# Kernel optimization log

Hardware: AMD Instinct MI355X
Metric: run time of the kernel (lower is better)

The kernel has to match this reference:

```python
import jax, jax.numpy as jnp
import numpy as np

B, L, HID, TRANS = 16384, 512, 768, 128


def setup_inputs() -> dict:
    key = jax.random.key(0)
    ks = jax.random.split(key, 12)
    def lin(k, out_d, in_d):
        kw, kb = jax.random.split(k)
        s = 1.0 / np.sqrt(in_d)
        return (jax.random.uniform(kw, (out_d, in_d), jnp.float32, -s, s),
                jax.random.uniform(kb, (out_d,), jnp.float32, -s, s))
    W_text, b_text = lin(ks[0], TRANS, HID)
    W_label, b_label = lin(ks[1], TRANS, HID)
    W0, b0 = lin(ks[2], TRANS, 2 * TRANS)
    W1, b1 = lin(ks[3], TRANS, TRANS)
    W2, b2 = lin(ks[4], 1, TRANS)
    target = jax.random.randint(ks[5], (B, L), 0, 2, jnp.int32)
    # guarantee every sample has at least one positive label (torch.mean on empty would NaN)
    target = target.at[:, 0].set(1)
    return {
        "text_embed": jax.random.normal(ks[6], (B, HID), jnp.float32),
        "label_embed": jax.random.normal(ks[7], (L, HID), jnp.float32),
        "target": target,
        "perm": jax.random.permutation(ks[8], B).astype(jnp.int32),
        "W_text": W_text, "b_text": b_text,
        "W_label": W_label, "b_label": b_label,
        "W0": W0, "b0": b0, "W1": W1, "b1": b1, "W2": W2, "b2": b2,
    }


def _network(t, l, W_text, b_text, W_label, b_label, W0, b0, W1, b1, W2, b2):
    tt = t @ W_text.T + b_text            # [B, trans]
    ll = l @ W_label.T + b_label          # [B, trans]
    h = jnp.concatenate([tt, ll], axis=1)  # [B, 2*trans]
    h = jax.nn.relu(h @ W0.T + b0)
    h = jax.nn.relu(h @ W1.T + b1)
    return h @ W2.T + b2                  # [B, 1]


def reference(text_embed, label_embed, target, perm,
              W_text, b_text, W_label, b_label, W0, b0, W1, b1, W2, b2):
    # variable-length mean pooling of label embeddings selected by the multi-hot target
    mask = target.astype(text_embed.dtype)                 # [B, L]
    counts = jnp.maximum(mask.sum(axis=1, keepdims=True), 1.0)
    label_feature_y = (mask @ label_embed) / counts        # [B, hid]
    negative_text = text_embed[perm]                       # shuffled negatives
    params = (W_text, b_text, W_label, b_label, W0, b0, W1, b1, W2, b2)
    E_joint = -jnp.mean(jax.nn.softplus(-_network(text_embed, label_feature_y, *params)))
    E_marginal = jnp.mean(jax.nn.softplus(_network(negative_text, label_feature_y, *params)))
    return E_marginal - E_joint
```

## Files before the change

### kernel.cpp

```cpp
#include <hip/hip_runtime.h>
#include <math.h>

#define BATCH 16384
#define LBL   512
#define HID   768
#define TR    128

typedef unsigned long long u64;
typedef unsigned short ushort_t;
typedef __attribute__((ext_vector_type(8))) short short8;
typedef __attribute__((ext_vector_type(4))) float f32x4;

__device__ __forceinline__ ushort_t f2bf(float f){
  unsigned u = __builtin_bit_cast(unsigned, f);
  u += 0x7FFFu + ((u >> 16) & 1u);
  return (ushort_t)(u >> 16);
}
__device__ __forceinline__ float softplusf(float x){
  return fmaxf(x, 0.0f) + log1pf(expf(-fabsf(x)));
}
__device__ __forceinline__ void gload_lds16(const void* g, void* l){
  __builtin_amdgcn_global_load_lds((const __attribute__((address_space(1))) void*)g,
                                   (__attribute__((address_space(3))) void*)l, 16, 0, 0);
}

__global__ __launch_bounds__(256) void k1(
    const float* __restrict__ W0, const float* __restrict__ Wt, const float* __restrict__ Wl,
    const float* __restrict__ bt, const float* __restrict__ bl, const float* __restrict__ b0,
    const float* __restrict__ W1,
    ushort_t* __restrict__ Msw, ushort_t* __restrict__ Qsw, ushort_t* __restrict__ W1B,
    float* __restrict__ KV, float* __restrict__ out){
  __shared__ float sw[TR];
  int bi = blockIdx.x, t = threadIdx.x;
  if (bi < 256){
    int i = bi & 127;
    int isQ = bi >> 7;
    const float* src = isQ ? Wl : Wt;
    ushort_t* dst = isQ ? Qsw : Msw;
    if (t < TR) sw[t] = W0[(size_t)i*256 + isQ*128 + t];
    if (!isQ && t < 128) W1B[i*128 + t] = f2bf(W1[i*128 + t]);
    __syncthreads();
    int c = t;
    float a0 = 0.f, a1 = 0.f, a2 = 0.f;
    #pragma unroll 8
    for (int a = 0; a < 128; a++){
      float w = sw[a];
      const float* r = src + (size_t)a*HID;
      a0 = fmaf(w, r[c], a0);
      a1 = fmaf(w, r[c+256], a1);
      a2 = fmaf(w, r[c+512], a2);
    }
    int c7 = c & 7;
    dst[(((c      )>>3)<<10) + (i<<3) + c7] = f2bf(a0);
    dst[(((c + 256)>>3)<<10) + (i<<3) + c7] = f2bf(a1);
    dst[(((c + 512)>>3)<<10) + (i<<3) + c7] = f2bf(a2);
  } else {
    if (t < TR){
      float s = b0[t];
      const float* r = W0 + (size_t)t*256;
      for (int a = 0; a < 128; a++) s = fmaf(r[a], bt[a], s);
      for (int a = 0; a < 128; a++) s = fmaf(r[128+a], bl[a], s);
      KV[t] = s;
    }
    if (t == 0) out[0] = 0.f;
  }
}

__device__ __forceinline__ void gemm768_32(const float* ap, const ushort_t* Bsw,
                                           ushort_t* As_, ushort_t* Bs_,
                                           int tid, int wave, int m, int q,
                                           f32x4 acc[2][2]){
  float4 ra0 = *(const float4*)ap;
  float4 ra1 = *(const float4*)(ap + 4);
  {
    const char* gb = (const char*)Bsw;
    char* lb = (char*)Bs_;
    #pragma unroll
    for (int p = 0; p < 4; p++)
      gload_lds16(gb + p*4096 + tid*16, lb + p*4096 + tid*16);
  }
  #pragma unroll
  for (int rt = 0; rt < 2; rt++)
    #pragma unroll
    for (int ct = 0; ct < 2; ct++)
      acc[rt][ct] = (f32x4){0.f,0.f,0.f,0.f};

  for (int c = 0; c < 12; c++){
    int buf = c & 1;
    short8 av;
    av[0] = (short)f2bf(ra0.x); av[1] = (short)f2bf(ra0.y);
    av[2] = (short)f2bf(ra0.z); av[3] = (short)f2bf(ra0.w);
    av[4] = (short)f2bf(ra1.x); av[5] = (short)f2bf(ra1.y);
    av[6] = (short)f2bf(ra1.z); av[7] = (short)f2bf(ra1.w);
    *(short8*)(As_ + (size_t)(buf*32 + (tid >> 3))*80 + (tid & 7)*8) = av;
    __syncthreads();
    if (c < 11){
      ra0 = *(const float4*)(ap + (c+1)*64);
      ra1 = *(const float4*)(ap + (c+1)*64 + 4);
      const char* gb = (const char*)Bsw + (size_t)(c+1)*16384;
      char* lb = (char*)(Bs_ + (buf^1)*8192);
      #pragma unroll
      for (int p = 0; p < 4; p++)
        gload_lds16(gb + p*4096 + tid*16, lb + p*4096 + tid*16);
    }
    #pragma unroll
    for (int kcc = 0; kcc < 2; kcc++){
      short8 bfr[2];
      #pragma unroll
      for (int ct = 0; ct < 2; ct++)
        bfr[ct] = *(const short8*)(Bs_ + buf*8192 + (kcc*4 + q)*1024 + (wave*32 + ct*16 + m)*8);
      #pragma unroll
      for (int rt = 0; rt < 2; rt++){
        short8 a = *(const short8*)(As_ + (size_t)(buf*32 + rt*16 + m)*80 + kcc*32 + q*8);
        #pragma unroll
        for (int ct = 0; ct < 2; ct++)
          acc[rt][ct] = __builtin_amdgcn_mfma_f32_16x16x32_bf16(a, bfr[ct], acc[rt][ct], 0, 0, 0);
      }
    }
  }
}

__global__ __launch_bounds__(256) void k2(
    const float* __restrict__ labe, const ushort_t* __restrict__ Qsw,
    ushort_t* __restrict__ Gt){
  __shared__ __align__(16) char uni[43008];
  int bi = blockIdx.x, tid = threadIdx.x;
  int lane = tid & 63, wave = tid >> 6;
  int m = lane & 15, q = lane >> 4;
  ushort_t* Bs_ = (ushort_t*)uni;
  ushort_t* As_ = (ushort_t*)(uni + 32768);

  int l0 = bi * 32;
  int arow = tid >> 3, ak = (tid & 7) * 8;
  f32x4 accG[2][2];
  gemm768_32(labe + (size_t)(l0 + arow)*HID + ak, Qsw, As_, Bs_, tid, wave, m, q, accG);
  __syncthreads();
  ushort_t (*GTs)[40] = (ushort_t(*)[40])uni;
  #pragma unroll
  for (int rt = 0; rt < 2; rt++)
    #pragma unroll
    for (int ct = 0; ct < 2; ct++){
      int col = wave*32 + ct*16 + m;
      #pragma unroll
      for (int r = 0; r < 4; r++)
        GTs[col][rt*16 + q*4 + r] = f2bf(accG[rt][ct][r]);
    }
  __syncthreads();
  int gi = tid >> 1, half = tid & 1;
  ushort_t* dstp = Gt + (size_t)gi*LBL + l0 + half*16;
  *(short8*)(dstp)     = *(const short8*)&GTs[gi][half*16];
  *(short8*)(dstp + 8) = *(const short8*)&GTs[gi][half*16 + 8];
}

__global__ __launch_bounds__(512, 4) void k3(const float* __restrict__ T, const ushort_t* __restrict__ Msw,
                                          const float* __restrict__ KV, const ushort_t* __restrict__ Gt,
                                          const int* __restrict__ tgt,
                                          const int* __restrict__ perm, const ushort_t* __restrict__ W1b,
                                          const float* __restrict__ b1, const float* __restrict__ W2,
                                          const float* __restrict__ b2, float* __restrict__ out){
  __shared__ __align__(16) char uni[51200];
  __shared__ __align__(16) u64 bitsS[32*10];
  __shared__ float invs[32];

  int tid = threadIdx.x;
  int lane = tid & 63, wave = tid >> 6;
  int m = lane & 15, q = lane >> 4;
  int r0 = blockIdx.x * 32;
  ushort_t* Bs_ = (ushort_t*)uni;
  ushort_t* As_ = (ushort_t*)(uni + 32768);

  int ar = tid >> 3, ak = (tid & 7) * 8;
  int arow = (ar < 32) ? (r0 + ar) : perm[r0 + ar - 32];
  const float* app = T + (size_t)arow*HID + ak;

  float4 a0 = *(const float4*)(app);
  float4 a1 = *(const float4*)(app + 4);
  {
    const char* gb = (const char*)Msw;
    char* lb = (char*)Bs_;
    gload_lds16(gb + tid*16,        lb + tid*16);
    gload_lds16(gb + 8192 + tid*16, lb + 8192 + tid*16);
  }
  int v[4][8];
  #pragma unroll
  for (int rr = 0; rr < 4; rr++){
    const int* rp = tgt + (size_t)(r0 + wave*4 + rr)*LBL;
    #pragma unroll
    for (int cc = 0; cc < 8; cc++) v[rr][cc] = rp[cc*64 + lane];
  }

  f32x4 acc[4];
  #pragma unroll
  for (int rt = 0; rt < 4; rt++) acc[rt] = (f32x4){0.f,0.f,0.f,0.f};

  for (int c = 0; c < 12; c++){
    int buf = c & 1;
    short8 av;
    av[0]=(short)f2bf(a0.x); av[1]=(short)f2bf(a0.y); av[2]=(short)f2bf(a0.z); av[3]=(short)f2bf(a0.w);
    av[4]=(short)f2bf(a1.x); av[5]=(short)f2bf(a1.y); av[6]=(short)f2bf(a1.z); av[7]=(short)f2bf(a1.w);
    *(short8*)(As_ + (size_t)(buf*64 + ar)*72 + ak) = av;
    __syncthreads();
    if (c == 8){
      #pragma unroll
      for (int rr = 0; rr < 4; rr++){
        int row = wave*4 + rr;
        int cnt = 0;
        #pragma unroll
        for (int cc = 0; cc < 8; cc++){
          u64 mm = __ballot(v[rr][cc] != 0);
          if (lane == 0){ ((u64*)((char*)bitsS + row*80))[cc] = mm; cnt += __popcll(mm); }
        }
        if (lane == 0) invs[row] = 1.0f / (float)(cnt < 1 ? 1 : cnt);
      }
    }
    if (c < 11){
      a0 = *(const float4*)(app + (c+1)*64);
      a1 = *(const float4*)(app + (c+1)*64 + 4);
      const char* gb = (const char*)Msw + (size_t)(c+1)*16384;
      char* lb = (char*)(Bs_ + (buf^1)*8192);
      gload_lds16(gb + tid*16,        lb + tid*16);
      gload_lds16(gb + 8192 + tid*16, lb + 8192 + tid*16);
    }
    #pragma unroll
    for (int kcc = 0; kcc < 2; kcc++){
      short8 bfr = *(const short8*)(Bs_ + buf*8192 + (kcc*4 + q)*1024 + (wave*16 + m)*8);
      #pragma unroll
      for (int rt = 0; rt < 4; rt++){
        short8 a = *(const short8*)(As_ + (size_t)(buf*64 + rt*16 + m)*72 + kcc*32 + q*8);
        acc[rt] = __builtin_amdgcn_mfma_f32_16x16x32_bf16(a, bfr, acc[rt], 0, 0, 0);
      }
    }
  }

  const unsigned char* bits_b = (const unsigned char*)bitsS;
  f32x4 accV[2] = {{0,0,0,0},{0,0,0,0}};
  const ushort_t* gp = Gt + (size_t)(wave*16 + m)*LBL + q*8;
  short8 bv0 = *(const short8*)(gp);
  short8 bv1 = *(const short8*)(gp + 32);
  for (int c = 0; c < 16; c++){
    short8 bn = bv1;
    if (c < 14) bn = *(const short8*)(gp + (size_t)(c+2)*32);
    #pragma unroll
    for (int rt = 0; rt < 2; rt++){
      unsigned bb = bits_b[(rt*16 + m)*80 + c*4 + q];
      short8 a;
      #pragma unroll
      for (int j = 0; j < 8; j++) a[j] = (short)(((bb >> j) & 1u) ? 0x3F80 : 0);
      accV[rt] = __builtin_amdgcn_mfma_f32_16x16x32_bf16(a, bv0, accV[rt], 0, 0, 0);
    }
    bv0 = bv1; bv1 = bn;
  }

  __syncthreads();
  ushort_t (*h0s)[136] = (ushort_t(*)[136])uni;
  float* sred = (float*)(uni + 17408);
  int col = wave*16 + m;
  float kv = KV[col];
  #pragma unroll
  for (int rt = 0; rt < 2; rt++){
    #pragma unroll
    for (int r = 0; r < 4; r++){
      int rowl = rt*16 + q*4 + r;
      float vv = accV[rt][r] * invs[rowl] + kv;
      h0s[rowl][col]      = f2bf(fmaxf(acc[rt][r]   + vv, 0.f));
      h0s[32 + rowl][col] = f2bf(fmaxf(acc[rt+2][r] + vv, 0.f));
    }
  }
  __syncthreads();

  float w2c = W2[col], b1c = b1[col];
  float b2v = b2[0];
  #pragma unroll
  for (int rt2 = 0; rt2 < 4; rt2++){
    f32x4 accH = {0,0,0,0};
    #pragma unroll
    for (int kc = 0; kc < 4; kc++){
      short8 a = *(const short8*)&h0s[rt2*16 + m][kc*32 + q*8];
      short8 b = *(const short8*)(W1b + (size_t)col*TR + kc*32 + q*8);
      accH = __builtin_amdgcn_mfma_f32_16x16x32_bf16(a, b, accH, 0, 0, 0);
    }
    #pragma unroll
    for (int r = 0; r < 4; r++){
      float sp = w2c * fmaxf(accH[r] + b1c, 0.f);
      sred[(size_t)(rt2*16 + q*4 + r)*129 + col] = sp;
    }
  }
  __syncthreads();

  if (tid < 64){
    float s = b2v;
    #pragma unroll
    for (int n = 0; n < 128; n++) s += sred[(size_t)tid*129 + n];
    float val = (tid < 32) ? softplusf(-s) : softplusf(s);
    #pragma unroll
    for (int off = 32; off > 0; off >>= 1) val += __shfl_down(val, off);
    if (tid == 0) atomicAdd(out, val * (1.0f / (float)BATCH));
  }
}

extern "C" void kernel_launch(void* const* d_in, const int* in_sizes, int n_in,
                              void* d_out, int out_size, void* d_ws, size_t ws_size,
                              hipStream_t stream){
  const float* text = (const float*)d_in[0];
  const float* labe = (const float*)d_in[1];
  const int*   tgt  = (const int*)  d_in[2];
  const int*   perm = (const int*)  d_in[3];
  const float* Wt   = (const float*)d_in[4];
  const float* bt   = (const float*)d_in[5];
  const float* Wl   = (const float*)d_in[6];
  const float* bl   = (const float*)d_in[7];
  const float* W0   = (const float*)d_in[8];
  const float* b0   = (const float*)d_in[9];
  const float* W1   = (const float*)d_in[10];
  const float* b1   = (const float*)d_in[11];
  const float* W2   = (const float*)d_in[12];
  const float* b2   = (const float*)d_in[13];

  char* wsb = (char*)d_ws;
  size_t off = 0;
  auto alloc = [&](size_t bytes){
    size_t r = off;
    off += (bytes + 255) & ~(size_t)255;
    return r;
  };
  ushort_t* MSW = (ushort_t*)(wsb + alloc((size_t)TR*HID*2));
  ushort_t* QSW = (ushort_t*)(wsb + alloc((size_t)TR*HID*2));
  ushort_t* GT  = (ushort_t*)(wsb + alloc((size_t)TR*LBL*2));
  ushort_t* W1B = (ushort_t*)(wsb + alloc((size_t)TR*TR*2));
  float*    KV  = (float*)   (wsb + alloc((size_t)TR*4));
  float*    out = (float*)d_out;
  (void)ws_size; (void)in_sizes; (void)n_in; (void)out_size;

  k1<<<257, 256, 0, stream>>>(W0, Wt, Wl, bt, bl, b0, W1, MSW, QSW, W1B, KV, out);
  k2<<<16, 256, 0, stream>>>(labe, QSW, GT);
  k3<<<512, 512, 0, stream>>>(text, MSW, KV, GT, tgt, perm, W1B, b1, W2, b2, out);
}
```

Baseline: 166.5 us.

## Fuse label-projection kernel into prep kernel and deepen k3 A-operand prefetch

Removes the separate k2 launch and the precomputed Qsw buffer. The label-embedding GEMM is now computed in extra k1 blocks as labe·Wl^T followed by a small GEMM with the W0 right half, so G is produced in the same launch as the other preprocessing. In k3 the target bitmask ballot is moved before the main loop, and text rows are prefetched two chunks ahead. The loop also uses explicit waitcnt, barriers and setprio to overlap loads with MFMA. In exchange, the label GEMM is reordered, which slightly changes bf16 rounding, and k1 becomes longer and heavier.

```diff
diff --git a/kernel.cpp b/kernel.cpp
--- a/kernel.cpp
+++ b/kernel.cpp
@@ -16,6 +16,12 @@
   u += 0x7FFFu + ((u >> 16) & 1u);
   return (ushort_t)(u >> 16);
 }
+__device__ __forceinline__ short8 pack8(float4 x, float4 y){
+  short8 v;
+  v[0]=(short)f2bf(x.x); v[1]=(short)f2bf(x.y); v[2]=(short)f2bf(x.z); v[3]=(short)f2bf(x.w);
+  v[4]=(short)f2bf(y.x); v[5]=(short)f2bf(y.y); v[6]=(short)f2bf(y.z); v[7]=(short)f2bf(y.w);
+  return v;
+}
 __device__ __forceinline__ float softplusf(float x){
   return fmaxf(x, 0.0f) + log1pf(expf(-fabsf(x)));
 }
@@ -27,34 +33,32 @@
 __global__ __launch_bounds__(256) void k1(
     const float* __restrict__ W0, const float* __restrict__ Wt, const float* __restrict__ Wl,
     const float* __restrict__ bt, const float* __restrict__ bl, const float* __restrict__ b0,
-    const float* __restrict__ W1,
-    ushort_t* __restrict__ Msw, ushort_t* __restrict__ Qsw, ushort_t* __restrict__ W1B,
+    const float* __restrict__ W1, const float* __restrict__ labe,
+    ushort_t* __restrict__ Msw, ushort_t* __restrict__ W1B, ushort_t* __restrict__ Gt,
     float* __restrict__ KV, float* __restrict__ out){
-  __shared__ float sw[TR];
+  __shared__ __align__(16) char uni[50688];
   int bi = blockIdx.x, t = threadIdx.x;
-  if (bi < 256){
-    int i = bi & 127;
-    int isQ = bi >> 7;
-    const float* src = isQ ? Wl : Wt;
-    ushort_t* dst = isQ ? Qsw : Msw;
-    if (t < TR) sw[t] = W0[(size_t)i*256 + isQ*128 + t];
-    if (!isQ && t < 128) W1B[i*128 + t] = f2bf(W1[i*128 + t]);
+  if (bi < 128){
+    float* sw = (float*)uni;
+    int i = bi;
+    if (t < TR) sw[t] = W0[(size_t)i*256 + t];
+    if (t < 128) W1B[i*128 + t] = f2bf(W1[i*128 + t]);
     __syncthreads();
     int c = t;
     float a0 = 0.f, a1 = 0.f, a2 = 0.f;
     #pragma unroll 8
     for (int a = 0; a < 128; a++){
       float w = sw[a];
-      const float* r = src + (size_t)a*HID;
+      const float* r = Wt + (size_t)a*HID;
       a0 = fmaf(w, r[c], a0);
       a1 = fmaf(w, r[c+256], a1);
       a2 = fmaf(w, r[c+512], a2);
     }
     int c7 = c & 7;
-    dst[(((c      )>>3)<<10) + (i<<3) + c7] = f2bf(a0);
-    dst[(((c + 256)>>3)<<10) + (i<<3) + c7] = f2bf(a1);
-    dst[(((c + 512)>>3)<<10) + (i<<3) + c7] = f2bf(a2);
-  } else {
+    Msw[(((c      )>>3)<<10) + (i<<3) + c7] = f2bf(a0);
+    Msw[(((c + 256)>>3)<<10) + (i<<3) + c7] = f2bf(a1);
+    Msw[(((c + 512)>>3)<<10) + (i<<3) + c7] = f2bf(a2);
+  } else if (bi == 128){
     if (t < TR){
       float s = b0[t];
       const float* r = W0 + (size_t)t*256;
@@ -63,93 +67,106 @@
       KV[t] = s;
     }
     if (t == 0) out[0] = 0.f;
-  }
-}
-
-__device__ __forceinline__ void gemm768_32(const float* ap, const ushort_t* Bsw,
-                                           ushort_t* As_, ushort_t* Bs_,
-                                           int tid, int wave, int m, int q,
-                                           f32x4 acc[2][2]){
-  float4 ra0 = *(const float4*)ap;
-  float4 ra1 = *(const float4*)(ap + 4);
-  {
-    const char* gb = (const char*)Bsw;
-    char* lb = (char*)Bs_;
-    #pragma unroll
-    for (int p = 0; p < 4; p++)
-      gload_lds16(gb + p*4096 + tid*16, lb + p*4096 + tid*16);
-  }
-  #pragma unroll
-  for (int rt = 0; rt < 2; rt++)
-    #pragma unroll
-    for (int ct = 0; ct < 2; ct++)
-      acc[rt][ct] = (f32x4){0.f,0.f,0.f,0.f};
-
-  for (int c = 0; c < 12; c++){
-    int buf = c & 1;
-    short8 av;
-    av[0] = (short)f2bf(ra0.x); av[1] = (short)f2bf(ra0.y);
-    av[2] = (short)f2bf(ra0.z); av[3] = (short)f2bf(ra0.w);
-    av[4] = (short)f2bf(ra1.x); av[5] = (short)f2bf(ra1.y);
-    av[6] = (short)f2bf(ra1.z); av[7] = (short)f2bf(ra1.w);
-    *(short8*)(As_ + (size_t)(buf*32 + (tid >> 3))*80 + (tid & 7)*8) = av;
+  } else {
+    int gi = bi - 129, l0 = gi * 32;
+    int lane = t & 63, wave = t >> 6;
+    int m = lane & 15, q = lane >> 4;
+    ushort_t* Bs1 = (ushort_t*)uni;
+    ushort_t* As1 = (ushort_t*)(uni + 32768);
+    ushort_t* Pl  = (ushort_t*)(uni + 41984);
+
+    int ar = t >> 3, ak = (t & 7) * 8;
+    const float* apl = labe + (size_t)(l0 + ar)*HID + ak;
+    int aB = t & 127, kh = t >> 7;
+    const float* wlr = Wl + (size_t)aB*HID + kh*32;
+
+    float4 ra0 = *(const float4*)apl;
+    float4 ra1 = *(const float4*)(apl + 4);
+    f32x4 accP[2][2];
+    #pragma unroll
+    for (int rt = 0; rt < 2; rt++)
+      #pragma unroll
+      for (int ct = 0; ct < 2; ct++) accP[rt][ct] = (f32x4){0.f,0.f,0.f,0.f};
+
+    for (int c = 0; c < 12; c++){
+      int buf = c & 1;
+      #pragma unroll
+      for (int j = 0; j < 4; j++){
+        float4 w0v = *(const float4*)(wlr + c*64 + j*8);
+        float4 w1v = *(const float4*)(wlr + c*64 + j*8 + 4);
+        *(short8*)(Bs1 + buf*8192 + (kh*4 + j)*1024 + aB*8) = pack8(w0v, w1v);
+      }
+      *(short8*)(As1 + (size_t)(buf*32 + ar)*72 + ak) = pack8(ra0, ra1);
+      __syncthreads();
+      if (c < 11){
+        ra0 = *(const float4*)(apl + (c+1)*64);
+        ra1 = *(const float4*)(apl + (c+1)*64 + 4);
+      }
+      #pragma unroll
+      for (int kcc = 0; kcc < 2; kcc++){
+        short8 bfr[2];
+        #pragma unroll
+        for (int ct = 0; ct < 2; ct++)
+          bfr[ct] = *(const short8*)(Bs1 + buf*8192 + (kcc*4 + q)*1024 + (wave*32 + ct*16 + m)*8);
+        #pragma unroll
+        for (int rt = 0; rt < 2; rt++){
+          short8 a = *(const short8*)(As1 + (size_t)(buf*32 + rt*16 + m)*72 + kcc*32 + q*8);
+          #pragma unroll
+          for (int ct = 0; ct < 2; ct++)
+            accP[rt][ct] = __builtin_amdgcn_mfma_f32_16x16x32_bf16(a, bfr[ct], accP[rt][ct], 0, 0, 0);
+        }
+      }
+    }
+    #pragma unroll
+    for (int rt = 0; rt < 2; rt++)
+      #pragma unroll
+      for (int ct = 0; ct < 2; ct++){
+        int col = wave*32 + ct*16 + m;
+        #pragma unroll
+        for (int r = 0; r < 4; r++)
+          Pl[(size_t)(rt*16 + q*4 + r)*136 + col] = f2bf(accP[rt][ct][r]);
+      }
     __syncthreads();
-    if (c < 11){
-      ra0 = *(const float4*)(ap + (c+1)*64);
-      ra1 = *(const float4*)(ap + (c+1)*64 + 4);
-      const char* gb = (const char*)Bsw + (size_t)(c+1)*16384;
-      char* lb = (char*)(Bs_ + (buf^1)*8192);
-      #pragma unroll
-      for (int p = 0; p < 4; p++)
-        gload_lds16(gb + p*4096 + tid*16, lb + p*4096 + tid*16);
-    }
-    #pragma unroll
-    for (int kcc = 0; kcc < 2; kcc++){
+
+    int jB = t & 127, ah = t >> 7;
+    const float* w0r = W0 + (size_t)jB*256 + 128 + ah*64;
+    #pragma unroll
+    for (int g2 = 0; g2 < 8; g2++){
+      float4 u0 = *(const float4*)(w0r + g2*8);
+      float4 u1 = *(const float4*)(w0r + g2*8 + 4);
+      *(short8*)(Bs1 + (ah*8 + g2)*1024 + jB*8) = pack8(u0, u1);
+    }
+    __syncthreads();
+
+    f32x4 accG[2][2];
+    #pragma unroll
+    for (int rt = 0; rt < 2; rt++)
+      #pragma unroll
+      for (int ct = 0; ct < 2; ct++) accG[rt][ct] = (f32x4){0.f,0.f,0.f,0.f};
+    #pragma unroll
+    for (int kc = 0; kc < 4; kc++){
       short8 bfr[2];
       #pragma unroll
       for (int ct = 0; ct < 2; ct++)
-        bfr[ct] = *(const short8*)(Bs_ + buf*8192 + (kcc*4 + q)*1024 + (wave*32 + ct*16 + m)*8);
+        bfr[ct] = *(const short8*)(Bs1 + (kc*4 + q)*1024 + (wave*32 + ct*16 + m)*8);
       #pragma unroll
       for (int rt = 0; rt < 2; rt++){
-        short8 a = *(const short8*)(As_ + (size_t)(buf*32 + rt*16 + m)*80 + kcc*32 + q*8);
+        short8 a = *(const short8*)(Pl + (size_t)(rt*16 + m)*136 + kc*32 + q*8);
         #pragma unroll
         for (int ct = 0; ct < 2; ct++)
-          acc[rt][ct] = __builtin_amdgcn_mfma_f32_16x16x32_bf16(a, bfr[ct], acc[rt][ct], 0, 0, 0);
-      }
-    }
-  }
-}
-
-__global__ __launch_bounds__(256) void k2(
-    const float* __restrict__ labe, const ushort_t* __restrict__ Qsw,
-    ushort_t* __restrict__ Gt){
-  __shared__ __align__(16) char uni[43008];
-  int bi = blockIdx.x, tid = threadIdx.x;
-  int lane = tid & 63, wave = tid >> 6;
-  int m = lane & 15, q = lane >> 4;
-  ushort_t* Bs_ = (ushort_t*)uni;
-  ushort_t* As_ = (ushort_t*)(uni + 32768);
-
-  int l0 = bi * 32;
-  int arow = tid >> 3, ak = (tid & 7) * 8;
-  f32x4 accG[2][2];
-  gemm768_32(labe + (size_t)(l0 + arow)*HID + ak, Qsw, As_, Bs_, tid, wave, m, q, accG);
-  __syncthreads();
-  ushort_t (*GTs)[40] = (ushort_t(*)[40])uni;
-  #pragma unroll
-  for (int rt = 0; rt < 2; rt++)
-    #pragma unroll
-    for (int ct = 0; ct < 2; ct++){
-      int col = wave*32 + ct*16 + m;
-      #pragma unroll
-      for (int r = 0; r < 4; r++)
-        GTs[col][rt*16 + q*4 + r] = f2bf(accG[rt][ct][r]);
-    }
-  __syncthreads();
-  int gi = tid >> 1, half = tid & 1;
-  ushort_t* dstp = Gt + (size_t)gi*LBL + l0 + half*16;
-  *(short8*)(dstp)     = *(const short8*)&GTs[gi][half*16];
-  *(short8*)(dstp + 8) = *(const short8*)&GTs[gi][half*16 + 8];
+          accG[rt][ct] = __builtin_amdgcn_mfma_f32_16x16x32_bf16(a, bfr[ct], accG[rt][ct], 0, 0, 0);
+      }
+    }
+    #pragma unroll
+    for (int rt = 0; rt < 2; rt++)
+      #pragma unroll
+      for (int ct = 0; ct < 2; ct++){
+        int j = wave*32 + ct*16 + m;
+        #pragma unroll
+        for (int r = 0; r < 4; r++)
+          Gt[(size_t)j*LBL + l0 + rt*16 + q*4 + r] = f2bf(accG[rt][ct][r]);
+      }
+  }
 }
 
 __global__ __launch_bounds__(512, 4) void k3(const float* __restrict__ T, const ushort_t* __restrict__ Msw,
@@ -169,58 +186,63 @@
   ushort_t* Bs_ = (ushort_t*)uni;
   ushort_t* As_ = (ushort_t*)(uni + 32768);
 
-  int ar = tid >> 3, ak = (tid & 7) * 8;
-  int arow = (ar < 32) ? (r0 + ar) : perm[r0 + ar - 32];
-  const float* app = T + (size_t)arow*HID + ak;
-
-  float4 a0 = *(const float4*)(app);
-  float4 a1 = *(const float4*)(app + 4);
   {
     const char* gb = (const char*)Msw;
     char* lb = (char*)Bs_;
     gload_lds16(gb + tid*16,        lb + tid*16);
     gload_lds16(gb + 8192 + tid*16, lb + 8192 + tid*16);
   }
-  int v[4][8];
+  int vv[4][8];
   #pragma unroll
   for (int rr = 0; rr < 4; rr++){
     const int* rp = tgt + (size_t)(r0 + wave*4 + rr)*LBL;
     #pragma unroll
-    for (int cc = 0; cc < 8; cc++) v[rr][cc] = rp[cc*64 + lane];
+    for (int cc = 0; cc < 8; cc++) vv[rr][cc] = rp[cc*64 + lane];
+  }
+  int ar = tid >> 3, ak = (tid & 7) * 8;
+  int arow = (ar < 32) ? (r0 + ar) : perm[r0 + ar - 32];
+  const float* app = T + (size_t)arow*HID + ak;
+  float4 aa0[2], aa1[2];
+  aa0[0] = *(const float4*)(app);      aa1[0] = *(const float4*)(app + 4);
+  aa0[1] = *(const float4*)(app + 64); aa1[1] = *(const float4*)(app + 68);
+
+  #pragma unroll
+  for (int rr = 0; rr < 4; rr++){
+    int row = wave*4 + rr;
+    int cnt = 0;
+    #pragma unroll
+    for (int cc = 0; cc < 8; cc++){
+      u64 mm = __ballot(vv[rr][cc] != 0);
+      if (lane == 0){ ((u64*)((char*)bitsS + row*80))[cc] = mm; cnt += __popcll(mm); }
+    }
+    if (lane == 0) invs[row] = 1.0f / (float)(cnt < 1 ? 1 : cnt);
   }
 
   f32x4 acc[4];
   #pragma unroll
   for (int rt = 0; rt < 4; rt++) acc[rt] = (f32x4){0.f,0.f,0.f,0.f};
 
+  #pragma unroll
   for (int c = 0; c < 12; c++){
     int buf = c & 1;
-    short8 av;
-    av[0]=(short)f2bf(a0.x); av[1]=(short)f2bf(a0.y); av[2]=(short)f2bf(a0.z); av[3]=(short)f2bf(a0.w);
-    av[4]=(short)f2bf(a1.x); av[5]=(short)f2bf(a1.y); av[6]=(short)f2bf(a1.z); av[7]=(short)f2bf(a1.w);
-    *(short8*)(As_ + (size_t)(buf*64 + ar)*72 + ak) = av;
-    __syncthreads();
-    if (c == 8){
-      #pragma unroll
-      for (int rr = 0; rr < 4; rr++){
-        int row = wave*4 + rr;
-        int cnt = 0;
-        #pragma unroll
-        for (int cc = 0; cc < 8; cc++){
-          u64 mm = __ballot(v[rr][cc] != 0);
-          if (lane == 0){ ((u64*)((char*)bitsS + row*80))[cc] = mm; cnt += __popcll(mm); }
-        }
-        if (lane == 0) invs[row] = 1.0f / (float)(cnt < 1 ? 1 : cnt);
-      }
-    }
+    *(short8*)(As_ + (size_t)(buf*64 + ar)*72 + ak) = pack8(aa0[buf], aa1[buf]);
+    if (c < 10){
+      aa0[buf] = *(const float4*)(app + (c+2)*64);
+      aa1[buf] = *(const float4*)(app + (c+2)*64 + 4);
+    }
+    __builtin_amdgcn_sched_barrier(0);
+    if (c < 10) asm volatile("s_waitcnt vmcnt(2) lgkmcnt(0)" ::: "memory");
+    else        asm volatile("s_waitcnt vmcnt(0) lgkmcnt(0)" ::: "memory");
+    __builtin_amdgcn_s_barrier();
+    __builtin_amdgcn_sched_barrier(0);
     if (c < 11){
-      a0 = *(const float4*)(app + (c+1)*64);
-      a1 = *(const float4*)(app + (c+1)*64 + 4);
       const char* gb = (const char*)Msw + (size_t)(c+1)*16384;
       char* lb = (char*)(Bs_ + (buf^1)*8192);
       gload_lds16(gb + tid*16,        lb + tid*16);
       gload_lds16(gb + 8192 + tid*16, lb + 8192 + tid*16);
     }
+    __builtin_amdgcn_sched_barrier(0);
+    __builtin_amdgcn_s_setprio(1);
     #pragma unroll
     for (int kcc = 0; kcc < 2; kcc++){
       short8 bfr = *(const short8*)(Bs_ + buf*8192 + (kcc*4 + q)*1024 + (wave*16 + m)*8);
@@ -230,6 +252,7 @@
         acc[rt] = __builtin_amdgcn_mfma_f32_16x16x32_bf16(a, bfr, acc[rt], 0, 0, 0);
       }
     }
+    __builtin_amdgcn_s_setprio(0);
   }
 
   const unsigned char* bits_b = (const unsigned char*)bitsS;
@@ -261,9 +284,9 @@
     #pragma unroll
     for (int r = 0; r < 4; r++){
       int rowl = rt*16 + q*4 + r;
-      float vv = accV[rt][r] * invs[rowl] + kv;
-      h0s[rowl][col]      = f2bf(fmaxf(acc[rt][r]   + vv, 0.f));
-      h0s[32 + rowl][col] = f2bf(fmaxf(acc[rt+2][r] + vv, 0.f));
+      float vvv = accV[rt][r] * invs[rowl] + kv;
+      h0s[rowl][col]      = f2bf(fmaxf(acc[rt][r]   + vvv, 0.f));
+      h0s[32 + rowl][col] = f2bf(fmaxf(acc[rt+2][r] + vvv, 0.f));
     }
   }
   __syncthreads();
@@ -324,14 +347,12 @@
     return r;
   };
   ushort_t* MSW = (ushort_t*)(wsb + alloc((size_t)TR*HID*2));
-  ushort_t* QSW = (ushort_t*)(wsb + alloc((size_t)TR*HID*2));
   ushort_t* GT  = (ushort_t*)(wsb + alloc((size_t)TR*LBL*2));
   ushort_t* W1B = (ushort_t*)(wsb + alloc((size_t)TR*TR*2));
   float*    KV  = (float*)   (wsb + alloc((size_t)TR*4));
   float*    out = (float*)d_out;
   (void)ws_size; (void)in_sizes; (void)n_in; (void)out_size;
 
-  k1<<<257, 256, 0, stream>>>(W0, Wt, Wl, bt, bl, b0, W1, MSW, QSW, W1B, KV, out);
-  k2<<<16, 256, 0, stream>>>(labe, QSW, GT);
+  k1<<<145, 256, 0, stream>>>(W0, Wt, Wl, bt, bl, b0, W1, labe, MSW, W1B, GT, KV, out);
   k3<<<512, 512, 0, stream>>>(text, MSW, KV, GT, tgt, perm, W1B, b1, W2, b2, out);
 }
```

Result: no change. 168.9 us (+1.4%).

## Deepen A-prefetch in k3 and use packed bf16 conversion with manual waitcnt barriers

Applied to the files above, without the earlier changes.

Replaces the software f32-to-bf16 rounding with v_cvt_pk_bf16_f32 packed conversions in both GEMM loops. In k3, moves the target ballot/count work out of the main loop, prefetches the A rows two chunks ahead with a register double-buffer, fully unrolls the loop, and replaces __syncthreads with explicit s_waitcnt plus s_barrier under sched barriers so outstanding loads are not drained each iteration. MFMA sections are raised in wave priority. This aims to hide global-load latency and cut conversion ALU work, at the cost of more registers and fragile hand-set vmcnt counts.

```diff
diff --git a/kernel.cpp b/kernel.cpp
--- a/kernel.cpp
+++ b/kernel.cpp
@@ -15,6 +15,14 @@
   unsigned u = __builtin_bit_cast(unsigned, f);
   u += 0x7FFFu + ((u >> 16) & 1u);
   return (ushort_t)(u >> 16);
+}
+__device__ __forceinline__ short8 pack8_cvt(float4 x, float4 y){
+  union { short8 s; unsigned u[4]; } r;
+  asm("v_cvt_pk_bf16_f32 %0, %1, %2" : "=v"(r.u[0]) : "v"(x.x), "v"(x.y));
+  asm("v_cvt_pk_bf16_f32 %0, %1, %2" : "=v"(r.u[1]) : "v"(x.z), "v"(x.w));
+  asm("v_cvt_pk_bf16_f32 %0, %1, %2" : "=v"(r.u[2]) : "v"(y.x), "v"(y.y));
+  asm("v_cvt_pk_bf16_f32 %0, %1, %2" : "=v"(r.u[3]) : "v"(y.z), "v"(y.w));
+  return r.s;
 }
 __device__ __forceinline__ float softplusf(float x){
   return fmaxf(x, 0.0f) + log1pf(expf(-fabsf(x)));
@@ -87,12 +95,7 @@
 
   for (int c = 0; c < 12; c++){
     int buf = c & 1;
-    short8 av;
-    av[0] = (short)f2bf(ra0.x); av[1] = (short)f2bf(ra0.y);
-    av[2] = (short)f2bf(ra0.z); av[3] = (short)f2bf(ra0.w);
-    av[4] = (short)f2bf(ra1.x); av[5] = (short)f2bf(ra1.y);
-    av[6] = (short)f2bf(ra1.z); av[7] = (short)f2bf(ra1.w);
-    *(short8*)(As_ + (size_t)(buf*32 + (tid >> 3))*80 + (tid & 7)*8) = av;
+    *(short8*)(As_ + (size_t)(buf*32 + (tid >> 3))*80 + (tid & 7)*8) = pack8_cvt(ra0, ra1);
     __syncthreads();
     if (c < 11){
       ra0 = *(const float4*)(ap + (c+1)*64);
@@ -169,58 +172,63 @@
   ushort_t* Bs_ = (ushort_t*)uni;
   ushort_t* As_ = (ushort_t*)(uni + 32768);
 
-  int ar = tid >> 3, ak = (tid & 7) * 8;
-  int arow = (ar < 32) ? (r0 + ar) : perm[r0 + ar - 32];
-  const float* app = T + (size_t)arow*HID + ak;
-
-  float4 a0 = *(const float4*)(app);
-  float4 a1 = *(const float4*)(app + 4);
   {
     const char* gb = (const char*)Msw;
     char* lb = (char*)Bs_;
     gload_lds16(gb + tid*16,        lb + tid*16);
     gload_lds16(gb + 8192 + tid*16, lb + 8192 + tid*16);
   }
-  int v[4][8];
+  int vv[4][8];
   #pragma unroll
   for (int rr = 0; rr < 4; rr++){
     const int* rp = tgt + (size_t)(r0 + wave*4 + rr)*LBL;
     #pragma unroll
-    for (int cc = 0; cc < 8; cc++) v[rr][cc] = rp[cc*64 + lane];
+    for (int cc = 0; cc < 8; cc++) vv[rr][cc] = rp[cc*64 + lane];
+  }
+  int ar = tid >> 3, ak = (tid & 7) * 8;
+  int arow = (ar < 32) ? (r0 + ar) : perm[r0 + ar - 32];
+  const float* app = T + (size_t)arow*HID + ak;
+  float4 aa0[2], aa1[2];
+  aa0[0] = *(const float4*)(app);      aa1[0] = *(const float4*)(app + 4);
+  aa0[1] = *(const float4*)(app + 64); aa1[1] = *(const float4*)(app + 68);
+
+  #pragma unroll
+  for (int rr = 0; rr < 4; rr++){
+    int row = wave*4 + rr;
+    int cnt = 0;
+    #pragma unroll
+    for (int cc = 0; cc < 8; cc++){
+      u64 mm = __ballot(vv[rr][cc] != 0);
+      if (lane == 0){ ((u64*)((char*)bitsS + row*80))[cc] = mm; cnt += __popcll(mm); }
+    }
+    if (lane == 0) invs[row] = 1.0f / (float)(cnt < 1 ? 1 : cnt);
   }
 
   f32x4 acc[4];
   #pragma unroll
   for (int rt = 0; rt < 4; rt++) acc[rt] = (f32x4){0.f,0.f,0.f,0.f};
 
+  #pragma unroll
   for (int c = 0; c < 12; c++){
     int buf = c & 1;
-    short8 av;
-    av[0]=(short)f2bf(a0.x); av[1]=(short)f2bf(a0.y); av[2]=(short)f2bf(a0.z); av[3]=(short)f2bf(a0.w);
-    av[4]=(short)f2bf(a1.x); av[5]=(short)f2bf(a1.y); av[6]=(short)f2bf(a1.z); av[7]=(short)f2bf(a1.w);
-    *(short8*)(As_ + (size_t)(buf*64 + ar)*72 + ak) = av;
-    __syncthreads();
-    if (c == 8){
-      #pragma unroll
-      for (int rr = 0; rr < 4; rr++){
-        int row = wave*4 + rr;
-        int cnt = 0;
-        #pragma unroll
-        for (int cc = 0; cc < 8; cc++){
-          u64 mm = __ballot(v[rr][cc] != 0);
-          if (lane == 0){ ((u64*)((char*)bitsS + row*80))[cc] = mm; cnt += __popcll(mm); }
-        }
-        if (lane == 0) invs[row] = 1.0f / (float)(cnt < 1 ? 1 : cnt);
-      }
-    }
+    *(short8*)(As_ + (size_t)(buf*64 + ar)*72 + ak)      = pack8_cvt(aa0[buf], aa1[buf]);
+    if (c < 10){
+      aa0[buf] = *(const float4*)(app + (c+2)*64);
+      aa1[buf] = *(const float4*)(app + (c+2)*64 + 4);
+    }
+    __builtin_amdgcn_sched_barrier(0);
+    if (c < 10) asm volatile("s_waitcnt vmcnt(2) lgkmcnt(0)" ::: "memory");
+    else        asm volatile("s_waitcnt vmcnt(0) lgkmcnt(0)" ::: "memory");
+    __builtin_amdgcn_s_barrier();
+    __builtin_amdgcn_sched_barrier(0);
     if (c < 11){
-      a0 = *(const float4*)(app + (c+1)*64);
-      a1 = *(const float4*)(app + (c+1)*64 + 4);
       const char* gb = (const char*)Msw + (size_t)(c+1)*16384;
       char* lb = (char*)(Bs_ + (buf^1)*8192);
       gload_lds16(gb + tid*16,        lb + tid*16);
       gload_lds16(gb + 8192 + tid*16, lb + 8192 + tid*16);
     }
+    __builtin_amdgcn_sched_barrier(0);
+    __builtin_amdgcn_s_setprio(1);
     #pragma unroll
     for (int kcc = 0; kcc < 2; kcc++){
       short8 bfr = *(const short8*)(Bs_ + buf*8192 + (kcc*4 + q)*1024 + (wave*16 + m)*8);
@@ -230,6 +238,7 @@
         acc[rt] = __builtin_amdgcn_mfma_f32_16x16x32_bf16(a, bfr, acc[rt], 0, 0, 0);
       }
     }
+    __builtin_amdgcn_s_setprio(0);
   }
 
   const unsigned char* bits_b = (const unsigned char*)bitsS;
@@ -261,9 +270,9 @@
     #pragma unroll
     for (int r = 0; r < 4; r++){
       int rowl = rt*16 + q*4 + r;
-      float vv = accV[rt][r] * invs[rowl] + kv;
-      h0s[rowl][col]      = f2bf(fmaxf(acc[rt][r]   + vv, 0.f));
-      h0s[32 + rowl][col] = f2bf(fmaxf(acc[rt+2][r] + vv, 0.f));
+      float vvv = accV[rt][r] * invs[rowl] + kv;
+      h0s[rowl][col]      = f2bf(fmaxf(acc[rt][r]   + vvv, 0.f));
+      h0s[32 + rowl][col] = f2bf(fmaxf(acc[rt+2][r] + vvv, 0.f));
     }
   }
   __syncthreads();
```

After: 164.8 us. About the same (-1.0%).
